# Optimization experiments

Measured on AMD Instinct MI355X. Metric: run time of the kernel, lower is better.

## Reference

```python
import jax, jax.numpy as jnp
import numpy as np

NEG = -1e30  # log-space 'zero'


def setup_inputs() -> dict:
    N, T, IDIM, V, S = 16, 1024, 512, 4096, 128
    key = jax.random.key(0)
    k0, k1, k2, k3, k4 = jax.random.split(key, 5)
    hs = jax.random.normal(k0, (N, T, IDIM), dtype=jnp.float32)
    hlens = jax.random.randint(k1, (N,), T // 2, T + 1).astype(jnp.int32)
    ys = jax.random.randint(k2, (N, S), 1, V).astype(jnp.int32)  # labels exclude blank=0
    ylens = jax.random.randint(k3, (N,), S // 2, S + 1).astype(jnp.int32)
    W = jax.random.normal(k4, (V, IDIM), dtype=jnp.float32) * 0.02
    b = jnp.zeros((V,), dtype=jnp.float32)
    return {"hs": hs, "hlens": hlens, "ys": ys, "ylens": ylens, "W": W, "b": b}


def _ctc_loss(logp, hlens, ys, ylens):
    # logp: (N, T, V) log-softmax outputs; blank index = 0
    N, T, V = logp.shape
    S = ys.shape[1]
    L = 2 * S + 1
    # extended label sequence: blank, y1, blank, y2, ..., blank
    ext = jnp.zeros((N, L), dtype=ys.dtype).at[:, 1::2].set(ys)  # (N, L)
    s_idx = jnp.arange(L)
    ext_prev2 = jnp.pad(ext, ((0, 0), (2, 0)))[:, :L]
    allow_skip = (ext != 0) & (ext != ext_prev2) & (s_idx[None, :] >= 2)  # (N, L)
    Ln = 2 * ylens + 1  # valid extended length per sample

    lpT = jnp.swapaxes(logp, 0, 1)  # (T, N, V)

    # t = 0 init
    alpha0 = jnp.full((N, L), NEG, dtype=logp.dtype)
    alpha0 = alpha0.at[:, 0].set(lpT[0, :, 0])
    alpha0 = alpha0.at[:, 1].set(jnp.take_along_axis(lpT[0], ys[:, :1], axis=1)[:, 0])

    def step(alpha, xs):
        lp_t, t = xs  # lp_t: (N, V)
        lp_ext = jnp.take_along_axis(lp_t, ext, axis=1)  # (N, L)
        a1 = alpha
        a2 = jnp.pad(alpha, ((0, 0), (1, 0)), constant_values=NEG)[:, :L]
        a3 = jnp.pad(alpha, ((0, 0), (2, 0)), constant_values=NEG)[:, :L]
        a3 = jnp.where(allow_skip, a3, NEG)
        new = jnp.logaddexp(jnp.logaddexp(a1, a2), a3) + lp_ext
        new = jnp.where(s_idx[None, :] < Ln[:, None], new, NEG)
        alpha = jnp.where((t < hlens)[:, None], new, alpha)
        return alpha, None

    ts = jnp.arange(1, T, dtype=hlens.dtype)
    alpha, _ = jax.lax.scan(step, alpha0, (lpT[1:], ts))

    end1 = jnp.take_along_axis(alpha, (Ln - 1)[:, None], axis=1)[:, 0]
    end2 = jnp.take_along_axis(alpha, (Ln - 2)[:, None], axis=1)[:, 0]
    ll = jnp.logaddexp(end1, end2)  # (N,)
    per = jnp.where(ll > -1e29, -ll, 0.0)  # zero_infinity=True
    return jnp.sum(per) / N  # reduction='sum' then divided by len(hlens)


def reference(hs, hlens, ys, ylens, W, b):
    logits = jnp.einsum('nti,vi->ntv', hs, W) + b  # (N, T, V)
    logp = jax.nn.log_softmax(logits, axis=-1)
    return _ctc_loss(logp, hlens, ys, ylens)
```

## Files before the change

### kernel.cpp

```cpp
#include <hip/hip_runtime.h>
#include <cstdint>
#include <cstddef>

using short8_t = __attribute__((ext_vector_type(8))) short;
using f32x4    = __attribute__((ext_vector_type(4))) float;
typedef unsigned short bfu16;

constexpr int   Nn   = 16;
constexpr int   Tt   = 1024;
constexpr int   IDIM = 512;
constexpr int   Vv   = 4096;
constexpr int   Ss   = 128;
constexpr int   Ll   = 2 * Ss + 1;
constexpr int   LS   = 132;
constexpr float NEGV = -1e30f;
constexpr float L2E  = 1.4426950408889634f;
constexpr float LN2  = 0.6931471805599453f;

__device__ __forceinline__ float fexp2(float x) { return __builtin_amdgcn_exp2f(x); }
__device__ __forceinline__ float flog2(float x) { return __builtin_amdgcn_logf(x); }

__device__ __forceinline__ bfu16 f2bf(float f) {
  unsigned int x = __float_as_uint(f);
  x = x + 0x7fffu + ((x >> 16) & 1u);
  return (bfu16)(x >> 16);
}

__device__ __forceinline__ void async16(const void* g, void* l) {
  __builtin_amdgcn_global_load_lds(
      (__attribute__((address_space(1))) void*)(g),
      (__attribute__((address_space(3))) void*)(l), 16, 0, 0);
}

__global__ void convert_zero(const float4* __restrict__ hs4,
                             const float4* __restrict__ W4,
                             ushort4* __restrict__ hsb4,
                             ushort4* __restrict__ Wb4,
                             float* __restrict__ out) {
  if (blockIdx.x == 0 && threadIdx.x == 0) out[0] = 0.f;
  const int HS4 = (Nn * Tt * IDIM) / 4;
  const int TOT = HS4 + (Vv * IDIM) / 4;
  for (int i = blockIdx.x * 256 + threadIdx.x; i < TOT; i += gridDim.x * 256) {
    float4 f;
    if (i < HS4) f = hs4[i]; else f = W4[i - HS4];
    ushort4 o;
    o.x = f2bf(f.x); o.y = f2bf(f.y); o.z = f2bf(f.z); o.w = f2bf(f.w);
    if (i < HS4) hsb4[i] = o; else Wb4[i - HS4] = o;
  }
}

__global__ void build_labels(const int* __restrict__ ys,
                             int* __restrict__ labmap,
                             int* __restrict__ extidx,
                             int* __restrict__ skipflag) {
  const int n = blockIdx.x, tid = threadIdx.x;
  int* lm = labmap + n * Vv;
  for (int v = tid; v < Vv; v += 256) lm[v] = 0x7fffffff;
  __syncthreads();
  if (tid == 0) lm[0] = 0;
  if (tid < Ss) atomicMin(&lm[ys[n * Ss + tid]], tid + 1);
  __syncthreads();
  for (int s = tid; s < Ll; s += 256) {
    int v = (s & 1) ? ys[n * Ss + ((s - 1) >> 1)] : 0;
    extidx[n * Ll + s] = lm[v];
    int allow = 0;
    if ((s & 1) && s >= 3) allow = (v != ys[n * Ss + ((s - 3) >> 1)]) ? 1 : 0;
    skipflag[n * Ll + s] = allow;
  }
  __syncthreads();
  for (int v = tid; v < Vv; v += 256)
    if (lm[v] == 0x7fffffff) lm[v] = -1;
}

__global__ __launch_bounds__(512, 2) void gemm_lse(
    const bfu16* __restrict__ A,
    const bfu16* __restrict__ B,
    const float* __restrict__ bias,
    const int*   __restrict__ labmap,
    float* __restrict__ plab,
    float* __restrict__ psum) {
  __shared__ alignas(128) char ldsraw[131072];
  const int tid  = threadIdx.x;
  const int lane = tid & 63, wid = tid >> 6;
  const int wr = wid >> 2, wc = wid & 3;

  const int flat = blockIdx.x;
  const int wg   = (flat & 7) * 128 + (flat >> 3);
  const int bR = wg >> 4, bC = wg & 15;
  const int rowbase = bR * 256, colbase = bC * 256;

  f32x4 acc[8][4];
#pragma unroll
  for (int m = 0; m < 8; m++)
#pragma unroll
    for (int n = 0; n < 4; n++) {
      f32x4 z = {0.f, 0.f, 0.f, 0.f};
      acc[m][n] = z;
    }

  const int  sw  = wid & 3;
  const bool isB = wid >= 4;
  const char* gsrc0 = (const char*)(isB ? (const void*)B : (const void*)A)
      + (size_t)((isB ? colbase : rowbase) + sw * 64 + (lane >> 3)) * (IDIM * 2)
      + (((lane & 7) ^ ((lane >> 3) & 7)) * 16);
  char* ldst0 = ldsraw + (isB ? 32768 : 0) + sw * 8192;

  const int fr = lane & 15;
  const int g  = lane >> 4;
  const int fx = fr & 7;

  const int nsamp = bR >> 2;
  const int* lm = labmap + nsamp * Vv;
  float bc[4];
  int   slot[4];
#pragma unroll
  for (int n = 0; n < 4; n++) {
    int c = colbase + wc * 64 + n * 16 + fr;
    bc[n]   = bias[c];
    slot[n] = lm[c];
  }

  auto stage = [&](int b, int t) {
#pragma unroll
    for (int i = 0; i < 8; ++i)
      async16(gsrc0 + (size_t)t * 128 + i * 8192, ldst0 + b * 65536 + i * 1024);
  };

  stage(0, 0);
  asm volatile("s_waitcnt vmcnt(0)" ::: "memory");
  __builtin_amdgcn_s_barrier();

  int buf = 0;
  for (int t = 0; t < 8; ++t) {
    const char* Ab = ldsraw + buf * 65536;
    const char* Bb = Ab + 32768;
    if (t < 7) stage(buf ^ 1, t + 1);

    short8_t a0[4], a1[4], a2[4], a3[4], b0[4], b1[4];
#pragma unroll
    for (int m = 0; m < 4; m++)
      a0[m] = *(const short8_t*)(Ab + (wr * 128 + m * 16 + fr) * 128 + ((0 + g) ^ fx) * 16);
#pragma unroll
    for (int n = 0; n < 4; n++)
      b0[n] = *(const short8_t*)(Bb + (wc * 64 + n * 16 + fr) * 128 + ((0 + g) ^ fx) * 16);
#pragma unroll
    for (int m = 0; m < 4; m++)
      a1[m] = *(const short8_t*)(Ab + (wr * 128 + (m + 4) * 16 + fr) * 128 + ((0 + g) ^ fx) * 16);

    __builtin_amdgcn_s_setprio(1);
#pragma unroll
    for (int m = 0; m < 4; m++)
#pragma unroll
      for (int n = 0; n < 4; n++)
        acc[m][n] = __builtin_amdgcn_mfma_f32_16x16x32_bf16(a0[m], b0[n], acc[m][n], 0, 0, 0);
    __builtin_amdgcn_s_setprio(0);

#pragma unroll
    for (int m = 0; m < 4; m++)
      a2[m] = *(const short8_t*)(Ab + (wr * 128 + m * 16 + fr) * 128 + ((4 + g) ^ fx) * 16);
#pragma unroll
    for (int n = 0; n < 4; n++)
      b1[n] = *(const short8_t*)(Bb + (wc * 64 + n * 16 + fr) * 128 + ((4 + g) ^ fx) * 16);

    __builtin_amdgcn_s_setprio(1);
#pragma unroll
    for (int m = 0; m < 4; m++)
#pragma unroll
      for (int n = 0; n < 4; n++)
        acc[m + 4][n] = __builtin_amdgcn_mfma_f32_16x16x32_bf16(a1[m], b0[n], acc[m + 4][n], 0, 0, 0);
    __builtin_amdgcn_s_setprio(0);

#pragma unroll
    for (int m = 0; m < 4; m++)
      a3[m] = *(const short8_t*)(Ab + (wr * 128 + (m + 4) * 16 + fr) * 128 + ((4 + g) ^ fx) * 16);

    __builtin_amdgcn_s_setprio(1);
#pragma unroll
    for (int m = 0; m < 4; m++)
#pragma unroll
      for (int n = 0; n < 4; n++)
        acc[m][n] = __builtin_amdgcn_mfma_f32_16x16x32_bf16(a2[m], b1[n], acc[m][n], 0, 0, 0);
    __builtin_amdgcn_s_setprio(0);

    __builtin_amdgcn_s_setprio(1);
#pragma unroll
    for (int m = 0; m < 4; m++)
#pragma unroll
      for (int n = 0; n < 4; n++)
        acc[m + 4][n] = __builtin_amdgcn_mfma_f32_16x16x32_bf16(a3[m], b1[n], acc[m + 4][n], 0, 0, 0);
    __builtin_amdgcn_s_setprio(0);

    asm volatile("s_waitcnt vmcnt(0)" ::: "memory");
    __builtin_amdgcn_s_barrier();
    buf ^= 1;
  }

  const int g4 = g * 4;
#pragma unroll
  for (int m = 0; m < 8; m++) {
#pragma unroll
    for (int r = 0; r < 4; r++) {
      int row = rowbase + wr * 128 + m * 16 + g4 + r;
      float e0 = fexp2((acc[m][0][r] + bc[0]) * L2E);
      float e1 = fexp2((acc[m][1][r] + bc[1]) * L2E);
      float e2 = fexp2((acc[m][2][r] + bc[2]) * L2E);
      float e3 = fexp2((acc[m][3][r] + bc[3]) * L2E);
      if (slot[0] >= 0) plab[(size_t)row * LS + slot[0]] = e0;
      if (slot[1] >= 0) plab[(size_t)row * LS + slot[1]] = e1;
      if (slot[2] >= 0) plab[(size_t)row * LS + slot[2]] = e2;
      if (slot[3] >= 0) plab[(size_t)row * LS + slot[3]] = e3;
      float s = (e0 + e1) + (e2 + e3);
      s += __shfl_xor(s, 1);
      s += __shfl_xor(s, 2);
      s += __shfl_xor(s, 4);
      s += __shfl_xor(s, 8);
      if (fr == 0) {
        int pc = bC * 4 + wc;
        psum[(size_t)pc * 16384 + row] = s;
      }
    }
  }
}

__global__ void lse_reduce(const float* __restrict__ psum,
                           float* __restrict__ lse) {
  int row = blockIdx.x * 256 + threadIdx.x;
  float s = 0.f;
#pragma unroll 8
  for (int j = 0; j < 64; j++)
    s += psum[(size_t)j * 16384 + row];
  lse[row] = flog2(s) * LN2;
}

constexpr int BRK = 16;

__global__ __launch_bounds__(64) void ctc_dp(
    const float* __restrict__ plab, const float* __restrict__ lse,
    const int* __restrict__ extidx, const int* __restrict__ skipflag,
    const int* __restrict__ hlens, const int* __restrict__ ylens,
    float* __restrict__ out) {
  __shared__ float lbuf[2][2304];
  __shared__ float alf[264];
  const int n    = blockIdx.x;
  const int lane = threadIdx.x;
  const int hlen = hlens[n];
  const int Ln   = 2 * ylens[n] + 1;
  const int sbase = lane * 4;

  const int   e1  = extidx[n * Ll + sbase + 1];
  const int   e3  = extidx[n * Ll + sbase + 3];
  const float sk1 = skipflag[n * Ll + sbase + 1] ? 1.f : 0.f;
  const float sk3 = skipflag[n * Ll + sbase + 3] ? 1.f : 0.f;
  const float skh = (lane > 0 && skipflag[n * Ll + sbase - 1]) ? 1.f : 0.f;
  const bool  l0  = (lane == 0);
  const float m0  = (sbase + 0 < Ln) ? 1.f : 0.f;
  const float m1  = (sbase + 1 < Ln) ? 1.f : 0.f;
  const float m2  = (sbase + 2 < Ln) ? 1.f : 0.f;
  const float m3  = (sbase + 3 < Ln) ? 1.f : 0.f;
  const float m4  = (lane == 63 && Ln == 257) ? 1.f : 0.f;

  const float* pl  = plab + (size_t)n * Tt * LS;
  const float* lsp = lse + n * Tt;

  float slse = 0.f;
#pragma unroll
  for (int j = 0; j < 16; j++) {
    int t = lane + 64 * j;
    float v = lsp[t];
    slse += (t < hlen) ? v : 0.f;
  }
#pragma unroll
  for (int off = 32; off; off >>= 1) slse += __shfl_xor(slse, off);

  float a0 = 0.f, a1 = 0.f, a2 = 0.f, a3 = 0.f, a4 = 0.f;
  if (l0) { a0 = pl[0]; a1 = pl[e1]; }

  int sc = 0;

  auto pair2 = [&](float pbA, float p1A, float p3A,
                   float pbB, float p1B, float p3B) {
    float pa3 = __shfl_up(a3, 1);
    float pa2 = __shfl_up(a2, 1);
    float pa1 = __shfl_up(a1, 1);
    float prA = __shfl_up(p3A, 1);
    pa3 = l0 ? 0.f : pa3;
    pa2 = l0 ? 0.f : pa2;
    pa1 = l0 ? 0.f : pa1;
    float h1 = (pa3 + pa2 + skh * pa1) * prA;
    float s4 = (a4 + a3) * pbA;
    float s3 = (a3 + a2 + sk3 * a1) * p3A;
    float s2 = (a2 + a1) * pbA;
    float s1 = (a1 + a0 + sk1 * pa3) * p1A;
    float s0 = (a0 + pa3) * pbA;
    a4 = (s4 + s3) * pbB;
    a3 = (s3 + s2 + sk3 * s1) * p3B;
    a2 = (s2 + s1) * pbB;
    a1 = (s1 + s0 + sk1 * h1) * p1B;
    a0 = (s0 + h1) * pbB;
  };

  auto step1 = [&](float pb, float p1, float p3) {
    float pm1 = __shfl_up(a3, 1);
    pm1 = l0 ? 0.f : pm1;
    float n4 = (a4 + a3) * pb;
    float n3 = (a3 + a2 + sk3 * a1) * p3;
    float n2 = (a2 + a1) * pb;
    float n1 = (a1 + a0 + sk1 * pm1) * p1;
    float n0 = (a0 + pm1) * pb;
    a0 = n0; a1 = n1; a2 = n2; a3 = n3; a4 = n4;
  };

  auto rescale = [&]() {
    a0 *= m0; a1 *= m1; a2 *= m2; a3 *= m3; a4 *= m4;
    float mx = fmaxf(fmaxf(a0, a1), fmaxf(a2, a3));
    mx = fmaxf(mx, a4);
#pragma unroll
    for (int off = 32; off; off >>= 1) mx = fmaxf(mx, __shfl_xor(mx, off));
    int ee = (int)((__float_as_uint(mx) >> 23) & 0xff) - 127;
    ee = (mx > 0.f) ? ee : 0;
    float s = __uint_as_float((unsigned)(127 - ee) << 23);
    sc += ee;
    a0 *= s; a1 *= s; a2 *= s; a3 *= s; a4 *= s;
  };

  auto stageblk = [&](int bsel, int row0) {
    const char* src = (const char*)(pl + (size_t)row0 * LS);
    char* dst = (char*)&lbuf[bsel][0];
#pragma unroll
    for (int i = 0; i < 9; ++i)
      async16(src + i * 1024 + lane * 16, dst + i * 1024);
  };

  const int nsteps = hlen - 1;
  const int nblk   = nsteps / BRK;

  if (nblk > 0) {
    stageblk(0, 1);
    asm volatile("s_waitcnt vmcnt(0)" ::: "memory");
  }

  for (int b = 0; b < nblk; b++) {
    if (b + 1 < nblk) stageblk((b + 1) & 1, 1 + BRK * (b + 1));
    const float* Lb = &lbuf[b & 1][0];

    float gb[2], g1[2], g3[2], hb[2], h1v[2], h3[2];
    gb[0]  = Lb[0];         g1[0]  = Lb[e1];        g3[0]  = Lb[e3];
    hb[0]  = Lb[132];       h1v[0] = Lb[132 + e1];  h3[0]  = Lb[132 + e3];
#pragma unroll
    for (int d = 0; d < 8; d++) {
      if (d < 7) {
        const float* rA = Lb + (2 * d + 2) * 132;
        gb[(d + 1) & 1]  = rA[0];   g1[(d + 1) & 1]  = rA[e1];   g3[(d + 1) & 1]  = rA[e3];
        hb[(d + 1) & 1]  = rA[132]; h1v[(d + 1) & 1] = rA[132 + e1]; h3[(d + 1) & 1] = rA[132 + e3];
      }
      pair2(gb[d & 1], g1[d & 1], g3[d & 1], hb[d & 1], h1v[d & 1], h3[d & 1]);
    }
    rescale();
    asm volatile("s_waitcnt vmcnt(0)" ::: "memory");
  }

  int t = 1 + nblk * BRK;
  for (; t + 1 <= nsteps; t += 2) {
    pair2(pl[(size_t)t * LS], pl[(size_t)t * LS + e1], pl[(size_t)t * LS + e3],
          pl[(size_t)(t + 1) * LS], pl[(size_t)(t + 1) * LS + e1], pl[(size_t)(t + 1) * LS + e3]);
  }
  if (t <= nsteps) {
    step1(pl[(size_t)t * LS], pl[(size_t)t * LS + e1], pl[(size_t)t * LS + e3]);
  }
  rescale();

  alf[sbase + 0] = a0; alf[sbase + 1] = a1;
  alf[sbase + 2] = a2; alf[sbase + 3] = a3;
  if (lane == 63) alf[256] = a4;
  __syncthreads();
  if (l0) {
    float sum = alf[Ln - 1] + alf[Ln - 2];
    float per = 0.f;
    if (sum > 0.f) {
      float llv = (flog2(sum) + (float)sc) * LN2 - slse;
      if (llv > -1e29f) per = -llv;
    }
    atomicAdd(out, per * (1.0f / 16.0f));
  }
}

extern "C" void kernel_launch(void* const* d_in, const int* in_sizes, int n_in,
                              void* d_out, int out_size, void* d_ws, size_t ws_size,
                              hipStream_t stream) {
  const float* hs    = (const float*)d_in[0];
  const int*   hlens = (const int*)d_in[1];
  const int*   ys    = (const int*)d_in[2];
  const int*   ylens = (const int*)d_in[3];
  const float* W     = (const float*)d_in[4];
  const float* bias  = (const float*)d_in[5];
  float*       out   = (float*)d_out;
  char*        ws    = (char*)d_ws;

  const size_t off_hsb    = 0;
  const size_t off_Wb     = off_hsb    + (size_t)Nn*Tt*IDIM*2;
  const size_t off_plab   = off_Wb     + (size_t)Vv*IDIM*2;
  const size_t off_psum   = off_plab   + (size_t)Nn*Tt*LS*4;
  const size_t off_lse    = off_psum   + (size_t)64*16384*4;
  const size_t off_labmap = off_lse    + (size_t)16384*4;
  const size_t off_extidx = off_labmap + (size_t)Nn*Vv*4;
  const size_t off_skip   = off_extidx + (size_t)((Nn*Ll*4 + 255) & ~255);

  bfu16* hsb    = (bfu16*)(ws + off_hsb);
  bfu16* Wb     = (bfu16*)(ws + off_Wb);
  float* plab   = (float*)(ws + off_plab);
  float* psum   = (float*)(ws + off_psum);
  float* lse    = (float*)(ws + off_lse);
  int*   labmap = (int*)(ws + off_labmap);
  int*   extidx = (int*)(ws + off_extidx);
  int*   skipf  = (int*)(ws + off_skip);

  convert_zero<<<2048, 256, 0, stream>>>(
      (const float4*)hs, (const float4*)W, (ushort4*)hsb, (ushort4*)Wb, out);
  build_labels<<<16, 256, 0, stream>>>(ys, labmap, extidx, skipf);
  gemm_lse<<<1024, 512, 0, stream>>>(hsb, Wb, bias, labmap, plab, psum);
  lse_reduce<<<64, 256, 0, stream>>>(psum, lse);
  ctc_dp<<<16, 64, 0, stream>>>(plab, lse, extidx, skipf, hlens, ylens, out);
}
```

Before: 210.0 us.

## Advance CTC alpha recursion four timesteps per cross-lane exchange

Replaces the two-step pair update in the blocked CTC DP loop with a four-step update. Each step block now does one set of neighbour-lane shuffles, recomputes the halo states from lanes below locally, and then runs four local recurrence steps. This cuts the number of shuffle round trips on the serial critical path. Label-probability shuffles are precomputed while the next group of rows loads. Rescaling now happens every other block, which risks overflow in linear space and adds halo arithmetic and registers.

```diff
diff --git a/kernel.cpp b/kernel.cpp
--- a/kernel.cpp
+++ b/kernel.cpp
@@ -252,7 +252,10 @@
   const float sk1 = skipflag[n * Ll + sbase + 1] ? 1.f : 0.f;
   const float sk3 = skipflag[n * Ll + sbase + 3] ? 1.f : 0.f;
   const float skh = (lane > 0 && skipflag[n * Ll + sbase - 1]) ? 1.f : 0.f;
+  const float skz = (lane > 0 && skipflag[n * Ll + sbase - 3]) ? 1.f : 0.f;
+  const float skv = (lane > 1 && skipflag[n * Ll + sbase - 5]) ? 1.f : 0.f;
   const bool  l0  = (lane == 0);
+  const bool  l01 = (lane < 2);
   const float m0  = (sbase + 0 < Ln) ? 1.f : 0.f;
   const float m1  = (sbase + 1 < Ln) ? 1.f : 0.f;
   const float m2  = (sbase + 2 < Ln) ? 1.f : 0.f;
@@ -331,6 +334,61 @@
       async16(src + i * 1024 + lane * 16, dst + i * 1024);
   };
 
+  float rpb[2][4], rp1[2][4], rp3[2][4];
+  float rx3[2][3];
+  float rz1[2][2];
+  float rv3[2][1];
+
+  auto loadring = [&](int slot, const float* Lb, int q) {
+#pragma unroll
+    for (int r = 0; r < 4; r++) {
+      const float* base = Lb + (4 * q + r) * 132;
+      rpb[slot][r] = base[0];
+      rp1[slot][r] = base[e1];
+      rp3[slot][r] = base[e3];
+    }
+#pragma unroll
+    for (int r = 0; r < 3; r++) rx3[slot][r] = __shfl_up(rp3[slot][r], 1);
+#pragma unroll
+    for (int r = 0; r < 2; r++) rz1[slot][r] = __shfl_up(rp1[slot][r], 1);
+    rv3[slot][0] = __shfl_up(rp3[slot][0], 2);
+  };
+
+  auto quad4 = [&](int slot) {
+    float x0 = __shfl_up(a3, 1);
+    float y0 = __shfl_up(a2, 1);
+    float z0 = __shfl_up(a1, 1);
+    float w0 = __shfl_up(a0, 1);
+    float v0 = __shfl_up(a3, 2);
+    float u0 = __shfl_up(a2, 2);
+    float q0 = __shfl_up(a1, 2);
+    x0 = l0 ? 0.f : x0;  y0 = l0 ? 0.f : y0;
+    z0 = l0 ? 0.f : z0;  w0 = l0 ? 0.f : w0;
+    v0 = l01 ? 0.f : v0; u0 = l01 ? 0.f : u0; q0 = l01 ? 0.f : q0;
+
+    float v1 = (v0 + u0 + skv * q0) * rv3[slot][0];
+    float w1 = (w0 + v0) * rpb[slot][0];
+    float z1 = (z0 + w0 + skz * v0) * rz1[slot][0];
+    float y1 = (y0 + z0) * rpb[slot][0];
+    float x1 = (x0 + y0 + skh * z0) * rx3[slot][0];
+    float z2 = (z1 + w1 + skz * v1) * rz1[slot][1];
+    float y2 = (y1 + z1) * rpb[slot][1];
+    float x2 = (x1 + y1 + skh * z1) * rx3[slot][1];
+    float x3 = (x2 + y2 + skh * z2) * rx3[slot][2];
+
+    float xk[4] = {x0, x1, x2, x3};
+#pragma unroll
+    for (int r = 0; r < 4; r++) {
+      float pb = rpb[slot][r], p1 = rp1[slot][r], p3 = rp3[slot][r];
+      float n4 = (a4 + a3) * pb;
+      float n3 = (a3 + a2 + sk3 * a1) * p3;
+      float n2 = (a2 + a1) * pb;
+      float n1 = (a1 + a0 + sk1 * xk[r]) * p1;
+      float n0 = (a0 + xk[r]) * pb;
+      a0 = n0; a1 = n1; a2 = n2; a3 = n3; a4 = n4;
+    }
+  };
+
   const int nsteps = hlen - 1;
   const int nblk   = nsteps / BRK;
 
@@ -342,20 +400,13 @@
   for (int b = 0; b < nblk; b++) {
     if (b + 1 < nblk) stageblk((b + 1) & 1, 1 + BRK * (b + 1));
     const float* Lb = &lbuf[b & 1][0];
-
-    float gb[2], g1[2], g3[2], hb[2], h1v[2], h3[2];
-    gb[0]  = Lb[0];         g1[0]  = Lb[e1];        g3[0]  = Lb[e3];
-    hb[0]  = Lb[132];       h1v[0] = Lb[132 + e1];  h3[0]  = Lb[132 + e3];
-#pragma unroll
-    for (int d = 0; d < 8; d++) {
-      if (d < 7) {
-        const float* rA = Lb + (2 * d + 2) * 132;
-        gb[(d + 1) & 1]  = rA[0];   g1[(d + 1) & 1]  = rA[e1];   g3[(d + 1) & 1]  = rA[e3];
-        hb[(d + 1) & 1]  = rA[132]; h1v[(d + 1) & 1] = rA[132 + e1]; h3[(d + 1) & 1] = rA[132 + e3];
-      }
-      pair2(gb[d & 1], g1[d & 1], g3[d & 1], hb[d & 1], h1v[d & 1], h3[d & 1]);
-    }
-    rescale();
+    loadring(0, Lb, 0);
+#pragma unroll
+    for (int q = 0; q < 4; q++) {
+      if (q < 3) loadring((q + 1) & 1, Lb, q + 1);
+      quad4(q & 1);
+    }
+    if ((b & 1) || b == nblk - 1) rescale();
     asm volatile("s_waitcnt vmcnt(0)" ::: "memory");
   }
 
```

Measured after the change: 209.4 us (median of 2 runs). No clear change (-0.3%).
